# Kernel tuning notes

Measured on AMD Instinct MI355X. Metric: run time of the kernel, lower is better.

The kernel has to match this reference:

```python
import jax, jax.numpy as jnp
import numpy as np

N = 256        # SSM state size
D_MODEL = 2048 # number of independent channels sharing the kernel
L_MAX = 4096   # sequence length


def setup_inputs() -> dict:
    key = jax.random.key(0)
    k1, k2, k3, k4 = jax.random.split(key, 4)
    s = float(np.sqrt(N))
    # Stable A: eigenvalues with negative real part so A^l stays bounded after
    # bilinear discretization with step = 1/L.
    A = 0.5 * jax.random.normal(k1, (N, N), jnp.float32) / s - jnp.eye(N, dtype=jnp.float32)
    B = jax.random.normal(k2, (N, 1), jnp.float32) / s   # lecun-scale
    C = jax.random.normal(k3, (1, N), jnp.float32) / s
    D = jnp.ones((1,), jnp.float32)
    y = jax.random.normal(k4, (D_MODEL, L_MAX), jnp.float32)
    return {"y": y, "A": A, "B": B, "C": C, "D": D}


def _build_kernel(A, B, C, L, step):
    # Bilinear (Tustin) discretization, as in discretize_SSM.
    I = jnp.eye(A.shape[0], dtype=A.dtype)
    BL = jnp.linalg.inv(I - (step / 2.0) * A)
    Abar = BL @ (I + (step / 2.0) * A)
    Bbar = (BL * step) @ B                      # (N, 1)
    # K[l] = C @ Abar^l @ Bbar, computed as L matvecs via scan
    # (same math as the matrix_power loop, without O(L*N^3) cost).
    def step_fn(x, _):
        return Abar @ x, (C @ x)[0]
    _, K = jax.lax.scan(step_fn, Bbar[:, 0], None, length=L)
    return K                                     # (L,)


def _causal_conv(y, K):
    # mode='full' convolution truncated to first L samples == causal conv.
    L = y.shape[-1]
    n = 2 * L
    Yf = jnp.fft.rfft(y, n=n, axis=-1)           # (d_model, n//2+1)
    Kf = jnp.fft.rfft(K, n=n)                    # (n//2+1,)
    return jnp.fft.irfft(Yf * Kf, n=n, axis=-1)[..., :L]


def reference(y, A, B, C, D):
    L = y.shape[-1]
    K = _build_kernel(A, B, C, L, step=1.0 / L)
    return _causal_conv(y, K) + D * y
```

## Files before the change

kernel.cpp:

```cpp
#include <hip/hip_runtime.h>

#define N_ 256
#define L_ 4096
#define DM_ 2048
#define STEPF (1.0f / 4096.0f)
#define NW 10
#define NV 5
#define RQN 4608

typedef short bf16x8 __attribute__((ext_vector_type(8)));
typedef float f32x4 __attribute__((ext_vector_type(4)));
typedef unsigned int uint32;

__device__ __forceinline__ uint32 bf16rne(float f) {
    uint32 u = __builtin_bit_cast(uint32, f);
    return (u + 0x7FFFu + ((u >> 16) & 1u)) >> 16;
}
__device__ __forceinline__ float rdlane(float v, int l) {
    return __builtin_bit_cast(float, __builtin_amdgcn_readlane(__builtin_bit_cast(int, v), l));
}
__device__ __forceinline__ float hif(float x) {
    return __builtin_bit_cast(float, __builtin_bit_cast(uint32, x) & 0xFFFF0000u);
}
#define PK2(LO, HI) __builtin_amdgcn_perm(__builtin_bit_cast(uint32, (HI)), \
                                          __builtin_bit_cast(uint32, (LO)), 0x07060302u)

__global__ __launch_bounds__(1024) void k_build(const float* __restrict__ Araw,
                                                const float* __restrict__ Bv,
                                                const float* __restrict__ Cv,
                                                const float* __restrict__ yf,
                                                uint2* __restrict__ Rqg,
                                                uint4* __restrict__ ybf) {
    const int tid = threadIdx.x;
    if (blockIdx.x > 0) {
        const size_t base = (size_t)(blockIdx.x - 1) * 32768;
        const float4* yin = (const float4*)(yf + base);
        uint4* yo = ybf + base / 8;
#pragma unroll
        for (int i = 0; i < 4; ++i) {
            int c = i * 1024 + tid;
            float4 q0 = yin[2 * c], q1 = yin[2 * c + 1];
            uint4 o; o.x = PK2(q0.x, q0.y); o.y = PK2(q0.z, q0.w);
                     o.z = PK2(q1.x, q1.y); o.w = PK2(q1.z, q1.w);
            yo[c] = o;
        }
        return;
    }

    __shared__ float sm[39168];
    float* kry = sm;
    float* red = sm + 3840;
    float* Wl  = sm + 5888;
    float* Vt  = sm + 22528;
    float* Kf  = sm;

    const int j = tid & 255, seg = tid >> 8, lane = tid & 63;
    const int e = 64 * seg + lane;
    float a[64];

#define DOT64(S0, S1, VV) { \
    _Pragma("unroll") \
    for (int m = 0; m < 64; m += 2) { \
        S0 = fmaf(rdlane(VV, m), a[m], S0); \
        S1 = fmaf(rdlane(VV, m + 1), a[m + 1], S1); \
    } }

#pragma unroll
    for (int m = 0; m < 64; ++m) a[m] = Araw[(64 * seg + m) * 256 + j];
    if (tid < 256) kry[tid] = Cv[tid];
    __syncthreads();
    const float WSC = 4032.0f / 4096.0f;
    {
        float vv = kry[e];
        for (int n = 1; n < NW; ++n) {
            float s0 = 0.f, s1 = 0.f;
            DOT64(s0, s1, vv)
            float* rb = red + (n & 1) * 1024;
            rb[seg * 256 + j] = s0 + s1;
            __syncthreads();
            float sc = WSC / (float)n;
            vv = (rb[e] + rb[256 + e] + rb[512 + e] + rb[768 + e]) * sc;
            if (tid < 256)
                kry[n * 256 + tid] = (rb[tid] + rb[256 + tid] + rb[512 + tid] + rb[768 + tid]) * sc;
        }
    }
    __syncthreads();
    {
        float kj[NW];
#pragma unroll
        for (int n = 0; n < NW; ++n) kj[n] = kry[n * 256 + j];
#pragma unroll
        for (int u = 0; u < 16; ++u) {
            int q = seg + 4 * u;
            float c = (float)q * (1.0f / 63.0f);
            float h = kj[NW - 1];
#pragma unroll
            for (int n = NW - 2; n >= 0; --n) h = fmaf(c, h, kj[n]);
            Wl[q * 260 + j] = h;
        }
    }

    {
        const float4* Ar = (const float4*)(Araw + (size_t)j * 256 + 64 * seg);
#pragma unroll
        for (int m4 = 0; m4 < 16; ++m4) {
            float4 q4 = Ar[m4];
            a[4 * m4] = q4.x; a[4 * m4 + 1] = q4.y; a[4 * m4 + 2] = q4.z; a[4 * m4 + 3] = q4.w;
        }
    }
    const float ms = 0.5f * STEPF;
    const float bve = Bv[e];
    {
        float vv = bve;
        for (int it = 0; it < 2; ++it) {
            float s0 = 0.f, s1 = 0.f;
            DOT64(s0, s1, vv)
            float* rb = red + (it & 1) * 1024;
            rb[seg * 256 + j] = s0 + s1;
            __syncthreads();
            vv = fmaf(ms, rb[e] + rb[256 + e] + rb[512 + e] + rb[768 + e], bve);
            if (it == 1 && tid < 256) {
                float su = rb[tid] + rb[256 + tid] + rb[512 + tid] + rb[768 + tid];
                kry[tid] = STEPF * fmaf(ms, su, Bv[tid]);
            }
        }
    }
    __syncthreads();
    const float VSC = 63.0f / 4096.0f;
    {
        float vv = kry[e];
        for (int n = 1; n < NV; ++n) {
            float s0 = 0.f, s1 = 0.f;
            DOT64(s0, s1, vv)
            float* rb = red + (n & 1) * 1024;
            rb[seg * 256 + j] = s0 + s1;
            __syncthreads();
            float sc = VSC / (float)n;
            vv = (rb[e] + rb[256 + e] + rb[512 + e] + rb[768 + e]) * sc;
            if (tid < 256)
                kry[n * 256 + tid] = (rb[tid] + rb[256 + tid] + rb[512 + tid] + rb[768 + tid]) * sc;
        }
    }
    __syncthreads();
    {
        float kj[NV];
#pragma unroll
        for (int n = 0; n < NV; ++n) kj[n] = kry[n * 256 + j];
#pragma unroll
        for (int u = 0; u < 16; ++u) {
            int r = seg + 4 * u;
            float c = (float)r * (1.0f / 63.0f);
            float h = kj[NV - 1];
#pragma unroll
            for (int n = NV - 2; n >= 0; --n) h = fmaf(c, h, kj[n]);
            Vt[r * 260 + j] = h;
        }
    }
    __syncthreads();

    {
        const int wv = tid >> 6;
        const int qt = wv >> 2, rt = wv & 3;
        const int n16 = lane & 15, g4 = lane >> 4;
        const int q = 16 * qt + n16;
        const int r = 16 * rt + n16;
        f32x4 ac = (f32x4){0.f, 0.f, 0.f, 0.f};
        for (int s = 0; s < 8; ++s) {
            const int kk = 32 * s + 8 * g4;
            float4 w0 = *(const float4*)&Wl[q * 260 + kk];
            float4 w1 = *(const float4*)&Wl[q * 260 + kk + 4];
            float4 v0 = *(const float4*)&Vt[r * 260 + kk];
            float4 v1 = *(const float4*)&Vt[r * 260 + kk + 4];
            uint4 uh; uh.x = PK2(w0.x, w0.y); uh.y = PK2(w0.z, w0.w);
                      uh.z = PK2(w1.x, w1.y); uh.w = PK2(w1.z, w1.w);
            float l0 = w0.x - hif(w0.x), l1 = w0.y - hif(w0.y);
            float l2 = w0.z - hif(w0.z), l3 = w0.w - hif(w0.w);
            float l4 = w1.x - hif(w1.x), l5 = w1.y - hif(w1.y);
            float l6 = w1.z - hif(w1.z), l7 = w1.w - hif(w1.w);
            uint4 ul; ul.x = PK2(l0, l1); ul.y = PK2(l2, l3);
                      ul.z = PK2(l4, l5); ul.w = PK2(l6, l7);
            uint4 uv; uv.x = PK2(v0.x, v0.y); uv.y = PK2(v0.z, v0.w);
                      uv.z = PK2(v1.x, v1.y); uv.w = PK2(v1.z, v1.w);
            ac = __builtin_amdgcn_mfma_f32_16x16x32_bf16(__builtin_bit_cast(bf16x8, uh),
                                                         __builtin_bit_cast(bf16x8, uv), ac, 0, 0, 0);
            ac = __builtin_amdgcn_mfma_f32_16x16x32_bf16(__builtin_bit_cast(bf16x8, ul),
                                                         __builtin_bit_cast(bf16x8, uv), ac, 0, 0, 0);
        }
#pragma unroll
        for (int jj = 0; jj < 4; ++jj)
            Kf[(16 * qt + 4 * g4 + jj) * 64 + r] = ac[jj];
    }
    __syncthreads();

    for (int i = tid; i < RQN; i += 1024) {
        int aa = 4095 - i;
        uint32 e0 = (aa >= 0) ? bf16rne(Kf[aa]) : 0u;
        uint32 e1 = (aa >= 1) ? bf16rne(Kf[aa - 1]) : 0u;
        uint32 e2 = (aa >= 2) ? bf16rne(Kf[aa - 2]) : 0u;
        uint32 e3 = (aa >= 3) ? bf16rne(Kf[aa - 3]) : 0u;
        uint2 v; v.x = e0 | (e1 << 16); v.y = e2 | (e3 << 16);
        Rqg[i] = v;
    }
#undef DOT64
}

__global__ __launch_bounds__(256, 2) void k_conv(const uint2* __restrict__ Rqg,
                                                 const uint4* __restrict__ ybf,
                                                 const float* __restrict__ y,
                                                 const float* __restrict__ Dp,
                                                 float* __restrict__ out) {
    __shared__ uint2 Rq[RQN];
    __shared__ f32x4 mbuf[2][8][64];
    const int tid = threadIdx.x;
#pragma unroll
    for (int i = 0; i < RQN / 256; ++i) Rq[i * 256 + tid] = Rqg[i * 256 + tid];
    __syncthreads();

    const int w = tid >> 6, lane = tid & 63;
    const int n = lane & 15, g = lane >> 4;
    const int ds = w & 1, jh = w >> 1;
    const int by = (int)blockIdx.y;
    const int d0w = (int)blockIdx.x * 32 + ds * 16;
    const int d = d0w + n;
    const uint4* __restrict__ ybr = ybf + (size_t)d * (L_ / 8);
    const float D0 = Dp[0];

#define LOADF(SL, I0) { \
    uint2 u0 = Rq[(I0)]; uint2 u1 = Rq[(I0) + 4]; \
    uint4 uu; uu.x = u0.x; uu.y = u0.y; uu.z = u1.x; uu.w = u1.y; \
    fr[SL] = __builtin_bit_cast(bf16x8, uu); }
#define MF(TI, SL) acc[TI] = __builtin_amdgcn_mfma_f32_16x16x32_bf16(av, fr[SL], acc[TI], 0, 0, 0);

#define STEPE(S0,S1,S2,S3,S4,S5,S6,S7,S8,S9,S10,S11,S12,S13,S14,S15) { \
    av = __builtin_bit_cast(bf16x8, ave); \
    MF(14, S14) MF(15, S15) \
    LOADF(S14, bcur + 32) LOADF(S15, bcur + 16) \
    ave = ybr[yn & 511]; \
    yn += 4; bcur += 32; \
    MF(0,S0) MF(1,S1) MF(2,S2) MF(3,S3) MF(4,S4) MF(5,S5) MF(6,S6) MF(7,S7) \
    MF(8,S8) MF(9,S9) MF(10,S10) MF(11,S11) MF(12,S12) MF(13,S13) \
}
#define STEPO(S0,S1,S2,S3,S4,S5,S6,S7,S8,S9,S10,S11,S12,S13,S14,S15) { \
    av = __builtin_bit_cast(bf16x8, avo); \
    MF(14, S14) MF(15, S15) \
    LOADF(S14, bcur + 32) LOADF(S15, bcur + 16) \
    avo = ybr[yn & 511]; \
    yn += 4; bcur += 32; \
    MF(0,S0) MF(1,S1) MF(2,S2) MF(3,S3) MF(4,S4) MF(5,S5) MF(6,S6) MF(7,S7) \
    MF(8,S8) MF(9,S9) MF(10,S10) MF(11,S11) MF(12,S12) MF(13,S13) \
}

#define ROUND8() \
    STEPE(0,1,2,3,4,5,6,7,8,9,10,11,12,13,14,15) \
    STEPO(14,15,0,1,2,3,4,5,6,7,8,9,10,11,12,13) \
    STEPE(12,13,14,15,0,1,2,3,4,5,6,7,8,9,10,11) \
    STEPO(10,11,12,13,14,15,0,1,2,3,4,5,6,7,8,9) \
    STEPE(8,9,10,11,12,13,14,15,0,1,2,3,4,5,6,7) \
    STEPO(6,7,8,9,10,11,12,13,14,15,0,1,2,3,4,5) \
    STEPE(4,5,6,7,8,9,10,11,12,13,14,15,0,1,2,3) \
    STEPO(2,3,4,5,6,7,8,9,10,11,12,13,14,15,0,1)

#define ROUND4() \
    STEPE(0,1,2,3,4,5,6,7,8,9,10,11,12,13,14,15) \
    STEPO(14,15,0,1,2,3,4,5,6,7,8,9,10,11,12,13) \
    STEPE(12,13,14,15,0,1,2,3,4,5,6,7,8,9,10,11) \
    STEPO(10,11,12,13,14,15,0,1,2,3,4,5,6,7,8,9)

    for (int strip = 0; strip < 2; ++strip) {
        const int v = strip ? by : (15 - by);
        const int t0 = v << 8;
        const int Sh = 4 * (v + 1);
        const int s0 = jh * Sh;

        f32x4 acc[16];
#pragma unroll
        for (int i = 0; i < 16; ++i) acc[i] = (f32x4){0.f, 0.f, 0.f, 0.f};
        bf16x8 fr[16], av;
        uint4 ave, avo;

        const int B0 = 4095 - t0 - n + 8 * g + 32 * s0;
#pragma unroll
        for (int ti = 0; ti < 16; ++ti) LOADF(ti, B0 - 16 * ti)
        ave = ybr[4 * s0 + g];
        avo = ybr[4 * s0 + 4 + g];
        int bcur = B0;
        int yn = 4 * s0 + 8 + g;

        const int n8 = Sh >> 3;
        for (int it = 0; it < n8; ++it) {
            ROUND8()
        }
        if (Sh & 4) {
            ROUND4()
        }

#pragma unroll
        for (int rr = 0; rr < 2; ++rr) {
            if (jh == 1) {
#pragma unroll
                for (int i = 0; i < 8; ++i) mbuf[ds][i][lane] = acc[rr * 8 + i];
            }
            __syncthreads();
            if (jh == 0) {
#pragma unroll
                for (int i = 0; i < 8; ++i) {
                    f32x4 m = mbuf[ds][i][lane];
                    acc[rr * 8 + i][0] += m[0]; acc[rr * 8 + i][1] += m[1];
                    acc[rr * 8 + i][2] += m[2]; acc[rr * 8 + i][3] += m[3];
                }
            }
            __syncthreads();
        }
        if (jh == 0) {
#pragma unroll
            for (int ti = 0; ti < 16; ++ti) {
                int tcol = t0 + 16 * ti + n;
#pragma unroll
                for (int r = 0; r < 4; ++r) {
                    int dr = d0w + 4 * g + r;
                    size_t ix = (size_t)dr * L_ + tcol;
                    out[ix] = acc[ti][r] + D0 * y[ix];
                }
            }
        }
    }

#undef ROUND8
#undef ROUND4
#undef STEPE
#undef STEPO
#undef MF
#undef LOADF
}


extern "C" void kernel_launch(void* const* d_in, const int* in_sizes, int n_in,
                              void* d_out, int out_size, void* d_ws, size_t ws_size,
                              hipStream_t stream) {
    const float* y  = (const float*)d_in[0];
    const float* A  = (const float*)d_in[1];
    const float* Bv = (const float*)d_in[2];
    const float* Cv = (const float*)d_in[3];
    const float* Dp = (const float*)d_in[4];
    float* out = (float*)d_out;
    char* w = (char*)d_ws;
    uint2* Rqg = (uint2*)w;
    uint4* ybf = (uint4*)(w + 36864);

    k_build<<<dim3(257), dim3(1024), 0, stream>>>(A, Bv, Cv, y, Rqg, ybf);
    k_conv<<<dim3(64, 8), dim3(256), 0, stream>>>(Rqg, ybf, y, Dp, out);

    (void)in_sizes; (void)n_in; (void)out_size; (void)ws_size;
}
```

Measured before the change: 68.31 us.

## Retile causal conv into 192-column strips plus split tail block

```diff
diff --git a/kernel.cpp b/kernel.cpp
--- a/kernel.cpp
+++ b/kernel.cpp
@@ -99,7 +99,6 @@
             Wl[q * 260 + j] = h;
         }
     }
-
     {
         const float4* Ar = (const float4*)(Araw + (size_t)j * 256 + 64 * seg);
 #pragma unroll
@@ -157,7 +156,6 @@
         }
     }
     __syncthreads();
-
     {
         const int wv = tid >> 6;
         const int qt = wv >> 2, rt = wv & 3;
@@ -191,7 +189,6 @@
             Kf[(16 * qt + 4 * g4 + jj) * 64 + r] = ac[jj];
     }
     __syncthreads();
-
     for (int i = tid; i < RQN; i += 1024) {
         int aa = 4095 - i;
         uint32 e0 = (aa >= 0) ? bf16rne(Kf[aa]) : 0u;
@@ -204,13 +201,13 @@
 #undef DOT64
 }
 
-__global__ __launch_bounds__(256, 2) void k_conv(const uint2* __restrict__ Rqg,
+__global__ __launch_bounds__(256, 4) void k_conv(const uint2* __restrict__ Rqg,
                                                  const uint4* __restrict__ ybf,
                                                  const float* __restrict__ y,
                                                  const float* __restrict__ Dp,
                                                  float* __restrict__ out) {
     __shared__ uint2 Rq[RQN];
-    __shared__ f32x4 mbuf[2][8][64];
+    __shared__ f32x4 mbuf[2][4][64];
     const int tid = threadIdx.x;
 #pragma unroll
     for (int i = 0; i < RQN / 256; ++i) Rq[i * 256 + tid] = Rqg[i * 256 + tid];
@@ -218,9 +215,10 @@
 
     const int w = tid >> 6, lane = tid & 63;
     const int n = lane & 15, g = lane >> 4;
-    const int ds = w & 1, jh = w >> 1;
     const int by = (int)blockIdx.y;
-    const int d0w = (int)blockIdx.x * 32 + ds * 16;
+    const int bx = (int)blockIdx.x;
+    const int ds = w & 1;
+    const int d0w = bx * 32 + ds * 16;
     const int d = d0w + n;
     const uint4* __restrict__ ybr = ybf + (size_t)d * (L_ / 8);
     const float D0 = Dp[0];
@@ -231,89 +229,129 @@
     fr[SL] = __builtin_bit_cast(bf16x8, uu); }
 #define MF(TI, SL) acc[TI] = __builtin_amdgcn_mfma_f32_16x16x32_bf16(av, fr[SL], acc[TI], 0, 0, 0);
 
-#define STEPE(S0,S1,S2,S3,S4,S5,S6,S7,S8,S9,S10,S11,S12,S13,S14,S15) { \
+    if (by == 0) {
+        const int h = w >> 1;
+        const int t0 = 3840 + 128 * h;
+        const int S = 124 + 4 * h;
+        f32x4 acc[8];
+#pragma unroll
+        for (int i = 0; i < 8; ++i) acc[i] = (f32x4){0.f, 0.f, 0.f, 0.f};
+        bf16x8 fr[8], av;
+        uint4 ave, avo;
+        const int B0 = 4095 - t0 - n + 8 * g;
+#pragma unroll
+        for (int ti = 0; ti < 8; ++ti) LOADF(ti, B0 - 16 * ti)
+        ave = ybr[g]; avo = ybr[4 + g];
+        int bcur = B0, yn = 8 + g;
+
+#define STEP8E(S0,S1,S2,S3,S4,S5,S6,S7) { \
     av = __builtin_bit_cast(bf16x8, ave); \
-    MF(14, S14) MF(15, S15) \
-    LOADF(S14, bcur + 32) LOADF(S15, bcur + 16) \
-    ave = ybr[yn & 511]; \
-    yn += 4; bcur += 32; \
-    MF(0,S0) MF(1,S1) MF(2,S2) MF(3,S3) MF(4,S4) MF(5,S5) MF(6,S6) MF(7,S7) \
-    MF(8,S8) MF(9,S9) MF(10,S10) MF(11,S11) MF(12,S12) MF(13,S13) \
-}
-#define STEPO(S0,S1,S2,S3,S4,S5,S6,S7,S8,S9,S10,S11,S12,S13,S14,S15) { \
+    MF(6, S6) MF(7, S7) \
+    LOADF(S6, bcur + 32) LOADF(S7, bcur + 16) \
+    ave = ybr[yn & 511]; yn += 4; bcur += 32; \
+    MF(0,S0) MF(1,S1) MF(2,S2) MF(3,S3) MF(4,S4) MF(5,S5) \
+}
+#define STEP8O(S0,S1,S2,S3,S4,S5,S6,S7) { \
     av = __builtin_bit_cast(bf16x8, avo); \
-    MF(14, S14) MF(15, S15) \
-    LOADF(S14, bcur + 32) LOADF(S15, bcur + 16) \
-    avo = ybr[yn & 511]; \
-    yn += 4; bcur += 32; \
-    MF(0,S0) MF(1,S1) MF(2,S2) MF(3,S3) MF(4,S4) MF(5,S5) MF(6,S6) MF(7,S7) \
-    MF(8,S8) MF(9,S9) MF(10,S10) MF(11,S11) MF(12,S12) MF(13,S13) \
-}
-
-#define ROUND8() \
-    STEPE(0,1,2,3,4,5,6,7,8,9,10,11,12,13,14,15) \
-    STEPO(14,15,0,1,2,3,4,5,6,7,8,9,10,11,12,13) \
-    STEPE(12,13,14,15,0,1,2,3,4,5,6,7,8,9,10,11) \
-    STEPO(10,11,12,13,14,15,0,1,2,3,4,5,6,7,8,9) \
-    STEPE(8,9,10,11,12,13,14,15,0,1,2,3,4,5,6,7) \
-    STEPO(6,7,8,9,10,11,12,13,14,15,0,1,2,3,4,5) \
-    STEPE(4,5,6,7,8,9,10,11,12,13,14,15,0,1,2,3) \
-    STEPO(2,3,4,5,6,7,8,9,10,11,12,13,14,15,0,1)
-
-#define ROUND4() \
-    STEPE(0,1,2,3,4,5,6,7,8,9,10,11,12,13,14,15) \
-    STEPO(14,15,0,1,2,3,4,5,6,7,8,9,10,11,12,13) \
-    STEPE(12,13,14,15,0,1,2,3,4,5,6,7,8,9,10,11) \
-    STEPO(10,11,12,13,14,15,0,1,2,3,4,5,6,7,8,9)
-
+    MF(6, S6) MF(7, S7) \
+    LOADF(S6, bcur + 32) LOADF(S7, bcur + 16) \
+    avo = ybr[yn & 511]; yn += 4; bcur += 32; \
+    MF(0,S0) MF(1,S1) MF(2,S2) MF(3,S3) MF(4,S4) MF(5,S5) \
+}
+        const int nr = S >> 2;
+        for (int it = 0; it < nr; ++it) {
+            STEP8E(0,1,2,3,4,5,6,7)
+            STEP8O(6,7,0,1,2,3,4,5)
+            STEP8E(4,5,6,7,0,1,2,3)
+            STEP8O(2,3,4,5,6,7,0,1)
+        }
+#undef STEP8E
+#undef STEP8O
+#pragma unroll
+        for (int ti = 0; ti < 8; ++ti) {
+            int tcol = t0 + 16 * ti + n;
+#pragma unroll
+            for (int r = 0; r < 4; ++r) {
+                int dr = d0w + 4 * g + r;
+                size_t ix = (size_t)dr * L_ + tcol;
+                out[ix] = acc[ti][r] + D0 * y[ix];
+            }
+        }
+        return;
+    }
+
+    const int jq = w >> 1;
     for (int strip = 0; strip < 2; ++strip) {
-        const int v = strip ? by : (15 - by);
-        const int t0 = v << 8;
-        const int Sh = 4 * (v + 1);
-        const int s0 = jh * Sh;
-
-        f32x4 acc[16];
-#pragma unroll
-        for (int i = 0; i < 16; ++i) acc[i] = (f32x4){0.f, 0.f, 0.f, 0.f};
-        bf16x8 fr[16], av;
+        const int v = strip ? (by - 1) : (20 - by);
+        const int t0 = 192 * v;
+        const int Sh = 3 * (v + 1);
+        const int s0 = jq * Sh;
+
+        f32x4 acc[12];
+#pragma unroll
+        for (int i = 0; i < 12; ++i) acc[i] = (f32x4){0.f, 0.f, 0.f, 0.f};
+        bf16x8 fr[12], av;
         uint4 ave, avo;
 
         const int B0 = 4095 - t0 - n + 8 * g + 32 * s0;
 #pragma unroll
-        for (int ti = 0; ti < 16; ++ti) LOADF(ti, B0 - 16 * ti)
-        ave = ybr[4 * s0 + g];
-        avo = ybr[4 * s0 + 4 + g];
-        int bcur = B0;
-        int yn = 4 * s0 + 8 + g;
-
-        const int n8 = Sh >> 3;
-        for (int it = 0; it < n8; ++it) {
-            ROUND8()
-        }
-        if (Sh & 4) {
-            ROUND4()
-        }
-
-#pragma unroll
-        for (int rr = 0; rr < 2; ++rr) {
-            if (jh == 1) {
-#pragma unroll
-                for (int i = 0; i < 8; ++i) mbuf[ds][i][lane] = acc[rr * 8 + i];
-            }
-            __syncthreads();
-            if (jh == 0) {
-#pragma unroll
-                for (int i = 0; i < 8; ++i) {
+        for (int ti = 0; ti < 12; ++ti) LOADF(ti, B0 - 16 * ti)
+        ave = ybr[(4 * s0 + g) & 511]; avo = ybr[(4 * s0 + 4 + g) & 511];
+        int bcur = B0, yn = 4 * s0 + 8 + g;
+
+#define STEP12E(S0,S1,S2,S3,S4,S5,S6,S7,S8,S9,S10,S11) { \
+    av = __builtin_bit_cast(bf16x8, ave); \
+    MF(10, S10) MF(11, S11) \
+    LOADF(S10, bcur + 32) LOADF(S11, bcur + 16) \
+    ave = ybr[yn & 511]; yn += 4; bcur += 32; \
+    MF(0,S0) MF(1,S1) MF(2,S2) MF(3,S3) MF(4,S4) MF(5,S5) \
+    MF(6,S6) MF(7,S7) MF(8,S8) MF(9,S9) \
+}
+#define STEP12O(S0,S1,S2,S3,S4,S5,S6,S7,S8,S9,S10,S11) { \
+    av = __builtin_bit_cast(bf16x8, avo); \
+    MF(10, S10) MF(11, S11) \
+    LOADF(S10, bcur + 32) LOADF(S11, bcur + 16) \
+    avo = ybr[yn & 511]; yn += 4; bcur += 32; \
+    MF(0,S0) MF(1,S1) MF(2,S2) MF(3,S3) MF(4,S4) MF(5,S5) \
+    MF(6,S6) MF(7,S7) MF(8,S8) MF(9,S9) \
+}
+        const int n6 = Sh / 6;
+        for (int it = 0; it < n6; ++it) {
+            STEP12E(0,1,2,3,4,5,6,7,8,9,10,11)
+            STEP12O(10,11,0,1,2,3,4,5,6,7,8,9)
+            STEP12E(8,9,10,11,0,1,2,3,4,5,6,7)
+            STEP12O(6,7,8,9,10,11,0,1,2,3,4,5)
+            STEP12E(4,5,6,7,8,9,10,11,0,1,2,3)
+            STEP12O(2,3,4,5,6,7,8,9,10,11,0,1)
+        }
+        if (Sh - 6 * n6) {
+            STEP12E(0,1,2,3,4,5,6,7,8,9,10,11)
+            STEP12O(10,11,0,1,2,3,4,5,6,7,8,9)
+            STEP12E(8,9,10,11,0,1,2,3,4,5,6,7)
+        }
+#undef STEP12E
+#undef STEP12O
+
+#pragma unroll
+        for (int rr = 0; rr < 3; ++rr) {
+            if (jq == 1) {
+#pragma unroll
+                for (int i = 0; i < 4; ++i) mbuf[ds][i][lane] = acc[4 * rr + i];
+            }
+            __syncthreads();
+            if (jq == 0) {
+#pragma unroll
+                for (int i = 0; i < 4; ++i) {
                     f32x4 m = mbuf[ds][i][lane];
-                    acc[rr * 8 + i][0] += m[0]; acc[rr * 8 + i][1] += m[1];
-                    acc[rr * 8 + i][2] += m[2]; acc[rr * 8 + i][3] += m[3];
+                    acc[4 * rr + i][0] += m[0]; acc[4 * rr + i][1] += m[1];
+                    acc[4 * rr + i][2] += m[2]; acc[4 * rr + i][3] += m[3];
                 }
             }
             __syncthreads();
         }
-        if (jh == 0) {
-#pragma unroll
-            for (int ti = 0; ti < 16; ++ti) {
+        if (jq == 0) {
+#pragma unroll
+            for (int ti = 0; ti < 12; ++ti) {
                 int tcol = t0 + 16 * ti + n;
 #pragma unroll
                 for (int r = 0; r < 4; ++r) {
@@ -324,11 +362,6 @@
             }
         }
     }
-
-#undef ROUND8
-#undef ROUND4
-#undef STEPE
-#undef STEPO
 #undef MF
 #undef LOADF
 }
@@ -348,7 +381,7 @@
     uint4* ybf = (uint4*)(w + 36864);
 
     k_build<<<dim3(257), dim3(1024), 0, stream>>>(A, Bv, Cv, y, Rqg, ybf);
-    k_conv<<<dim3(64, 8), dim3(256), 0, stream>>>(Rqg, ybf, y, Dp, out);
+    k_conv<<<dim3(64, 11), dim3(256), 0, stream>>>(Rqg, ybf, y, Dp, out);
 
     (void)in_sizes; (void)n_in; (void)out_size; (void)ws_size;
 }
```

After: 79.94 us. 17.0% more time.

## Switch conv to 32x32x16 MFMA with Toeplitz as A operand and swapped tiles

Applied to the files above, without the earlier changes.

```diff
diff --git a/kernel.cpp b/kernel.cpp
--- a/kernel.cpp
+++ b/kernel.cpp
@@ -10,6 +10,7 @@
 
 typedef short bf16x8 __attribute__((ext_vector_type(8)));
 typedef float f32x4 __attribute__((ext_vector_type(4)));
+typedef float f32x16 __attribute__((ext_vector_type(16)));
 typedef unsigned int uint32;
 
 __device__ __forceinline__ uint32 bf16rne(float f) {
@@ -99,7 +100,6 @@
             Wl[q * 260 + j] = h;
         }
     }
-
     {
         const float4* Ar = (const float4*)(Araw + (size_t)j * 256 + 64 * seg);
 #pragma unroll
@@ -157,7 +157,6 @@
         }
     }
     __syncthreads();
-
     {
         const int wv = tid >> 6;
         const int qt = wv >> 2, rt = wv & 3;
@@ -191,7 +190,6 @@
             Kf[(16 * qt + 4 * g4 + jj) * 64 + r] = ac[jj];
     }
     __syncthreads();
-
     for (int i = tid; i < RQN; i += 1024) {
         int aa = 4095 - i;
         uint32 e0 = (aa >= 0) ? bf16rne(Kf[aa]) : 0u;
@@ -217,11 +215,11 @@
     __syncthreads();
 
     const int w = tid >> 6, lane = tid & 63;
-    const int n = lane & 15, g = lane >> 4;
+    const int m32 = lane & 31, h = lane >> 5;
     const int ds = w & 1, jh = w >> 1;
     const int by = (int)blockIdx.y;
-    const int d0w = (int)blockIdx.x * 32 + ds * 16;
-    const int d = d0w + n;
+    const int d0w = (int)blockIdx.x * 64 + ds * 32;
+    const int d = d0w + m32;
     const uint4* __restrict__ ybr = ybf + (size_t)d * (L_ / 8);
     const float D0 = Dp[0];
 
@@ -229,107 +227,107 @@
     uint2 u0 = Rq[(I0)]; uint2 u1 = Rq[(I0) + 4]; \
     uint4 uu; uu.x = u0.x; uu.y = u0.y; uu.z = u1.x; uu.w = u1.y; \
     fr[SL] = __builtin_bit_cast(bf16x8, uu); }
-#define MF(TI, SL) acc[TI] = __builtin_amdgcn_mfma_f32_16x16x32_bf16(av, fr[SL], acc[TI], 0, 0, 0);
-
-#define STEPE(S0,S1,S2,S3,S4,S5,S6,S7,S8,S9,S10,S11,S12,S13,S14,S15) { \
-    av = __builtin_bit_cast(bf16x8, ave); \
-    MF(14, S14) MF(15, S15) \
-    LOADF(S14, bcur + 32) LOADF(S15, bcur + 16) \
-    ave = ybr[yn & 511]; \
-    yn += 4; bcur += 32; \
-    MF(0,S0) MF(1,S1) MF(2,S2) MF(3,S3) MF(4,S4) MF(5,S5) MF(6,S6) MF(7,S7) \
-    MF(8,S8) MF(9,S9) MF(10,S10) MF(11,S11) MF(12,S12) MF(13,S13) \
-}
-#define STEPO(S0,S1,S2,S3,S4,S5,S6,S7,S8,S9,S10,S11,S12,S13,S14,S15) { \
-    av = __builtin_bit_cast(bf16x8, avo); \
-    MF(14, S14) MF(15, S15) \
-    LOADF(S14, bcur + 32) LOADF(S15, bcur + 16) \
-    avo = ybr[yn & 511]; \
-    yn += 4; bcur += 32; \
-    MF(0,S0) MF(1,S1) MF(2,S2) MF(3,S3) MF(4,S4) MF(5,S5) MF(6,S6) MF(7,S7) \
-    MF(8,S8) MF(9,S9) MF(10,S10) MF(11,S11) MF(12,S12) MF(13,S13) \
+#define MFT(TT, SL) acc[TT] = __builtin_amdgcn_mfma_f32_32x32x16_bf16(fr[SL], bv, acc[TT], 0, 0, 0);
+
+#define STEPE(P) { \
+    bv = __builtin_bit_cast(bf16x8, ave); \
+    MFT(3, ((P) + 1) & 3) \
+    LOADF(((P) + 1) & 3, bcurE) bcurE += 32; \
+    ave = ybr[yn & 511]; yn += 2; \
+    MFT(0, (P) & 3) MFT(1, ((P) + 3) & 3) MFT(2, ((P) + 2) & 3) \
+}
+#define STEPO(P) { \
+    bv = __builtin_bit_cast(bf16x8, avo); \
+    MFT(3, 4 + (((P) + 1) & 3)) \
+    LOADF(4 + (((P) + 1) & 3), bcurO) bcurO += 32; \
+    avo = ybr[yn & 511]; yn += 2; \
+    MFT(0, 4 + ((P) & 3)) MFT(1, 4 + (((P) + 3) & 3)) MFT(2, 4 + (((P) + 2) & 3)) \
 }
 
 #define ROUND8() \
-    STEPE(0,1,2,3,4,5,6,7,8,9,10,11,12,13,14,15) \
-    STEPO(14,15,0,1,2,3,4,5,6,7,8,9,10,11,12,13) \
-    STEPE(12,13,14,15,0,1,2,3,4,5,6,7,8,9,10,11) \
-    STEPO(10,11,12,13,14,15,0,1,2,3,4,5,6,7,8,9) \
-    STEPE(8,9,10,11,12,13,14,15,0,1,2,3,4,5,6,7) \
-    STEPO(6,7,8,9,10,11,12,13,14,15,0,1,2,3,4,5) \
-    STEPE(4,5,6,7,8,9,10,11,12,13,14,15,0,1,2,3) \
-    STEPO(2,3,4,5,6,7,8,9,10,11,12,13,14,15,0,1)
-
-#define ROUND4() \
-    STEPE(0,1,2,3,4,5,6,7,8,9,10,11,12,13,14,15) \
-    STEPO(14,15,0,1,2,3,4,5,6,7,8,9,10,11,12,13) \
-    STEPE(12,13,14,15,0,1,2,3,4,5,6,7,8,9,10,11) \
-    STEPO(10,11,12,13,14,15,0,1,2,3,4,5,6,7,8,9)
+    STEPE(0) STEPO(0) STEPE(1) STEPO(1) STEPE(2) STEPO(2) STEPE(3) STEPO(3)
+#define REM4() \
+    STEPE(0) STEPO(0) STEPE(1) STEPO(1)
 
     for (int strip = 0; strip < 2; ++strip) {
-        const int v = strip ? by : (15 - by);
-        const int t0 = v << 8;
-        const int Sh = 4 * (v + 1);
-        const int s0 = jh * Sh;
-
-        f32x4 acc[16];
-#pragma unroll
-        for (int i = 0; i < 16; ++i) acc[i] = (f32x4){0.f, 0.f, 0.f, 0.f};
-        bf16x8 fr[16], av;
+        const int v = strip ? by : (31 - by);
+        const int t0 = v << 7;
+        const int Sh = 2 * (v + 1);
+        const int ShW = 4 * (v + 1);
+        const int s0 = jh * ShW;
+        (void)Sh;
+
+        f32x16 acc[4] = {};
+        bf16x8 fr[8], bv;
         uint4 ave, avo;
 
-        const int B0 = 4095 - t0 - n + 8 * g + 32 * s0;
-#pragma unroll
-        for (int ti = 0; ti < 16; ++ti) LOADF(ti, B0 - 16 * ti)
-        ave = ybr[4 * s0 + g];
-        avo = ybr[4 * s0 + 4 + g];
-        int bcur = B0;
-        int yn = 4 * s0 + 8 + g;
-
-        const int n8 = Sh >> 3;
+        const int IB = 4095 - t0 - m32 + 8 * h + 16 * s0;
+        LOADF(0, IB)      LOADF(3, IB - 32) LOADF(2, IB - 64) LOADF(1, IB - 96)
+        LOADF(4, IB + 16) LOADF(7, IB - 16) LOADF(6, IB - 48) LOADF(5, IB - 80)
+        ave = ybr[(2 * s0 + h) & 511];
+        avo = ybr[(2 * s0 + 2 + h) & 511];
+        int bcurE = IB + 32, bcurO = IB + 48;
+        int yn = 2 * s0 + 4 + h;
+
+        const int n8 = ShW >> 3;
         for (int it = 0; it < n8; ++it) {
             ROUND8()
         }
-        if (Sh & 4) {
-            ROUND4()
+        if (ShW & 4) {
+            REM4()
         }
 
 #pragma unroll
         for (int rr = 0; rr < 2; ++rr) {
             if (jh == 1) {
 #pragma unroll
-                for (int i = 0; i < 8; ++i) mbuf[ds][i][lane] = acc[rr * 8 + i];
+                for (int tp = 0; tp < 2; ++tp)
+#pragma unroll
+                    for (int c = 0; c < 4; ++c) {
+                        f32x4 ch = {acc[2 * rr + tp][4 * c], acc[2 * rr + tp][4 * c + 1],
+                                    acc[2 * rr + tp][4 * c + 2], acc[2 * rr + tp][4 * c + 3]};
+                        mbuf[ds][4 * tp + c][lane] = ch;
+                    }
             }
             __syncthreads();
             if (jh == 0) {
 #pragma unroll
-                for (int i = 0; i < 8; ++i) {
-                    f32x4 m = mbuf[ds][i][lane];
-                    acc[rr * 8 + i][0] += m[0]; acc[rr * 8 + i][1] += m[1];
-                    acc[rr * 8 + i][2] += m[2]; acc[rr * 8 + i][3] += m[3];
+                for (int tp = 0; tp < 2; ++tp)
+#pragma unroll
+                    for (int c = 0; c < 4; ++c) {
+                        f32x4 mm = mbuf[ds][4 * tp + c][lane];
+                        acc[2 * rr + tp][4 * c]     += mm[0];
+                        acc[2 * rr + tp][4 * c + 1] += mm[1];
+                        acc[2 * rr + tp][4 * c + 2] += mm[2];
+                        acc[2 * rr + tp][4 * c + 3] += mm[3];
+                    }
+            }
+            __syncthreads();
+        }
+        if (jh == 0) {
+#pragma unroll
+            for (int tt = 0; tt < 4; ++tt) {
+#pragma unroll
+                for (int q = 0; q < 4; ++q) {
+                    int tb = t0 + 32 * tt + 8 * q + 4 * h;
+                    size_t ix = (size_t)d * L_ + tb;
+                    float4 yv = *(const float4*)&y[ix];
+                    float4 o;
+                    o.x = acc[tt][4 * q]     + D0 * yv.x;
+                    o.y = acc[tt][4 * q + 1] + D0 * yv.y;
+                    o.z = acc[tt][4 * q + 2] + D0 * yv.z;
+                    o.w = acc[tt][4 * q + 3] + D0 * yv.w;
+                    *(float4*)&out[ix] = o;
                 }
             }
-            __syncthreads();
-        }
-        if (jh == 0) {
-#pragma unroll
-            for (int ti = 0; ti < 16; ++ti) {
-                int tcol = t0 + 16 * ti + n;
-#pragma unroll
-                for (int r = 0; r < 4; ++r) {
-                    int dr = d0w + 4 * g + r;
-                    size_t ix = (size_t)dr * L_ + tcol;
-                    out[ix] = acc[ti][r] + D0 * y[ix];
-                }
-            }
         }
     }
 
 #undef ROUND8
-#undef ROUND4
+#undef REM4
 #undef STEPE
 #undef STEPO
-#undef MF
+#undef MFT
 #undef LOADF
 }
 
@@ -348,7 +346,7 @@
     uint4* ybf = (uint4*)(w + 36864);
 
     k_build<<<dim3(257), dim3(1024), 0, stream>>>(A, Bv, Cv, y, Rqg, ybf);
-    k_conv<<<dim3(64, 8), dim3(256), 0, stream>>>(Rqg, ybf, y, Dp, out);
+    k_conv<<<dim3(32, 16), dim3(256), 0, stream>>>(Rqg, ybf, y, Dp, out);
 
     (void)in_sizes; (void)n_in; (void)out_size; (void)ws_size;
 }
```

After: 80.85 us. 18.4% more time.
